# Kernel optimization log

Measured on AMD Instinct MI355X. Metric: run time of the kernel, lower is better.

Reference implementation:

```python
import jax, jax.numpy as jnp
import numpy as np

T, STATE_DIM, ACTION_DIM = 1024, 1024, 64
D, S, H = 2048, 1024, 2048  # deterministic, stochastic, hidden (= embedding_size)


def _lin_init(k, out_dim, in_dim):
    k1, k2 = jax.random.split(k)
    lim = 1.0 / np.sqrt(in_dim)
    w = jax.random.uniform(k1, (out_dim, in_dim), minval=-lim, maxval=lim, dtype=jnp.float32)
    b = jax.random.uniform(k2, (out_dim,), minval=-lim, maxval=lim, dtype=jnp.float32)
    return w, b


def setup_inputs() -> dict:
    key = jax.random.key(0)
    ks = jax.random.split(key, 16)
    enc_w, enc_b = _lin_init(ks[0], H, STATE_DIM)                 # WorldModel.encoder
    dec_w, dec_b = _lin_init(ks[1], STATE_DIM + 2, S + D)         # WorldModel.decoder
    p_enc_w, p_enc_b = _lin_init(ks[2], D, S + ACTION_DIM)        # Prior.encoder
    glim = 1.0 / np.sqrt(D)
    gru_wih = jax.random.uniform(ks[3], (3 * D, D), minval=-glim, maxval=glim, dtype=jnp.float32)
    gru_whh = jax.random.uniform(ks[4], (3 * D, D), minval=-glim, maxval=glim, dtype=jnp.float32)
    gru_b = jax.random.uniform(ks[5], (3 * D,), minval=-glim, maxval=glim, dtype=jnp.float32)
    gru_bn = jax.random.uniform(ks[6], (D,), minval=-glim, maxval=glim, dtype=jnp.float32)
    p_dec1_w, p_dec1_b = _lin_init(ks[7], H, D)                   # Prior.decoder1
    p_dec2_w, p_dec2_b = _lin_init(ks[8], 2 * S, H)               # Prior.decoder2
    q_enc_w, q_enc_b = _lin_init(ks[9], H, D + H)                 # Posterior.encoder
    q_dec_w, q_dec_b = _lin_init(ks[10], 2 * S, H)                # Posterior.decoder
    observation = jax.random.normal(ks[11], (T, STATE_DIM), dtype=jnp.float32)
    actions = jax.random.normal(ks[12], (T, ACTION_DIM), dtype=jnp.float32)
    noise = jax.random.normal(ks[13], (T, S), dtype=jnp.float32)  # reparam eps for posterior sample
    return dict(observation=observation, actions=actions, noise=noise,
                enc_w=enc_w, enc_b=enc_b, dec_w=dec_w, dec_b=dec_b,
                p_enc_w=p_enc_w, p_enc_b=p_enc_b,
                gru_wih=gru_wih, gru_whh=gru_whh, gru_b=gru_b, gru_bn=gru_bn,
                p_dec1_w=p_dec1_w, p_dec1_b=p_dec1_b, p_dec2_w=p_dec2_w, p_dec2_b=p_dec2_b,
                q_enc_w=q_enc_w, q_enc_b=q_enc_b, q_dec_w=q_dec_w, q_dec_b=q_dec_b)


def reference(observation, actions, noise, enc_w, enc_b, dec_w, dec_b,
              p_enc_w, p_enc_b, gru_wih, gru_whh, gru_b, gru_bn,
              p_dec1_w, p_dec1_b, p_dec2_w, p_dec2_b,
              q_enc_w, q_enc_b, q_dec_w, q_dec_b):
    elu = jax.nn.elu
    # obs embeddings: [T, H]
    emb = elu(observation @ enc_w.T + enc_b)

    def step(carry, inp):
        stoch_prev, det_prev = carry
        e, act, eps = inp
        # Prior: encoder -> GRU -> decoder1 -> decoder2
        x = elu(p_enc_w @ jnp.concatenate([stoch_prev, act]) + p_enc_b)  # [D]
        ig = gru_wih @ x + gru_b
        hg = gru_whh @ det_prev
        ir, iz, inw = jnp.split(ig, 3)
        hr, hz, hn = jnp.split(hg, 3)
        r = jax.nn.sigmoid(ir + hr)
        z = jax.nn.sigmoid(iz + hz)
        n = jnp.tanh(inw + r * (hn + gru_bn))
        det = n + z * (det_prev - n)                                     # GRU hidden [D]
        y = elu(p_dec1_w @ det + p_dec1_b)
        y = p_dec2_w @ y + p_dec2_b
        pmu, pstd = jnp.split(y, 2)
        pstd = jax.nn.softplus(pstd) + 0.1
        # Posterior on (det, embedding)
        q = elu(q_enc_w @ jnp.concatenate([det, e]) + q_enc_b)
        q = q_dec_w @ q + q_dec_b
        qmu, qstd = jnp.split(q, 2)
        qstd = jax.nn.softplus(qstd) + 0.1
        stoch = qmu + qstd * eps                                         # Normal sample (reparam)
        return (stoch, det), (stoch, det, qmu, qstd, pmu, pstd)

    init = (jnp.zeros(S, observation.dtype), jnp.zeros(D, observation.dtype))
    _, (stoch, det, qmu, qstd, pmu, pstd) = jax.lax.scan(step, init, (emb, actions, noise))
    states_flat = jnp.concatenate([stoch, det], axis=-1)                  # [T, S+D]
    outs = states_flat @ dec_w.T + dec_b                                  # [T, state_dim+2]
    return stoch, det, outs, qmu, qstd, pmu, pstd


if __name__ == '__main__':
    out = reference(**setup_inputs())
    for o in out:
        print(o.shape)
```

## Files before the change

kernel.cpp:

```cpp
#include <hip/hip_runtime.h>
#include <cstdint>
#include <cstddef>

#define T_STEPS 1024
#define S_DIM   1024
#define A_DIM   64
#define D_DIM   2048
#define H_DIM   2048
#define NWG     256
#define NTHR    512

typedef unsigned short ushort_t;

__device__ __forceinline__ float eluf(float v)      { return v > 0.f ? v : expm1f(v); }
__device__ __forceinline__ float softplusf(float v) { return v > 20.f ? v : log1pf(expf(v)); }
__device__ __forceinline__ float sigmoidf_(float v) { return 1.f / (1.f + expf(-v)); }

__device__ __forceinline__ float wave_reduce(float v) {
  #pragma unroll
  for (int off = 32; off > 0; off >>= 1) v += __shfl_xor(v, off, 64);
  return v;
}

__device__ __forceinline__ float2 bf2(unsigned u) {
  float2 r;
  r.x = __uint_as_float(u << 16);
  r.y = __uint_as_float(u & 0xffff0000u);
  return r;
}
__device__ __forceinline__ ushort_t f2bf_rne(float f) {
  unsigned u = __float_as_uint(f);
  u += 0x7fffu + ((u >> 16) & 1u);
  return (ushort_t)(u >> 16);
}

#define LD_PIN_U4(dst, addr) \
  asm volatile("global_load_dwordx4 %0, %1, off" : "=v"(dst) : "v"(addr))

__device__ __forceinline__ void st_val(float* p, float v) {
  __hip_atomic_store((unsigned*)p, __float_as_uint(v),
                     __ATOMIC_RELAXED, __HIP_MEMORY_SCOPE_AGENT);
}
__device__ __forceinline__ void st_flag(unsigned* p, unsigned g) {
  __hip_atomic_store(p, g, __ATOMIC_RELAXED, __HIP_MEMORY_SCOPE_AGENT);
}

__device__ __forceinline__ void poll_flags(const unsigned* f, unsigned g, int lane) {
  const unsigned* p0 = f + (lane * 4 + 0) * 16;
  const unsigned* p1 = f + (lane * 4 + 1) * 16;
  const unsigned* p2 = f + (lane * 4 + 2) * 16;
  const unsigned* p3 = f + (lane * 4 + 3) * 16;
  for (;;) {
    unsigned a, b, c, d;
    asm volatile("global_load_dword %0, %4, off sc1\n\t"
                 "global_load_dword %1, %5, off sc1\n\t"
                 "global_load_dword %2, %6, off sc1\n\t"
                 "global_load_dword %3, %7, off sc1\n\t"
                 "s_waitcnt vmcnt(0)"
                 : "=v"(a), "=v"(b), "=v"(c), "=v"(d)
                 : "v"(p0), "v"(p1), "v"(p2), "v"(p3) : "memory");
    if (__all(a >= g && b >= g && c >= g && d >= g)) return;
    __builtin_amdgcn_s_sleep(1);
  }
}

__device__ __forceinline__ void bulk4(const float* __restrict__ src, int i4,
                                      float* __restrict__ lds) {
  float4 v;
  asm volatile("global_load_dwordx4 %0, %1, off sc1\n\ts_waitcnt vmcnt(0)"
               : "=v"(v) : "v"(src + i4) : "memory");
  *(float4*)(lds + i4) = v;
}

__global__ void init_flags(unsigned* f) {
  #pragma unroll
  for (int i = 0; i < 64; ++i) f[i * 256 + threadIdx.x] = 0u;
}

__global__ __launch_bounds__(256) void pack_lin(
    const float* __restrict__ src, unsigned* __restrict__ dst,
    int src_ld, int lc, size_t total_u32)
{
  for (size_t u = (size_t)blockIdx.x * 256 + threadIdx.x; u < total_u32;
       u += (size_t)gridDim.x * 256) {
    const size_t pos = u * 2;
    const size_t row = pos >> lc;
    const int    col = (int)(pos & (((size_t)1 << lc) - 1));
    const float2 v = *(const float2*)(src + row * src_ld + col);
    dst[u] = (unsigned)f2bf_rne(v.x) | ((unsigned)f2bf_rne(v.y) << 16);
  }
}

__global__ __launch_bounds__(256) void pack_swz(
    const float* __restrict__ src, unsigned* __restrict__ dst,
    int src_ld, int lc, size_t total2)
{
  for (size_t u = (size_t)blockIdx.x * 256 + threadIdx.x; u < total2;
       u += (size_t)gridDim.x * 256) {
    const size_t pos = u * 2;
    const size_t row = pos >> lc;
    const int pcol  = (int)(pos & (((size_t)1 << lc) - 1));
    const int chunk = pcol >> 9;
    const int off   = pcol & 511;
    const int l     = off >> 3;
    const int p     = (off >> 1) & 3;
    const float2 v  = *(const float2*)(src + row * src_ld + chunk * 512 + p * 128 + l * 2);
    dst[u] = (unsigned)f2bf_rne(v.x) | ((unsigned)f2bf_rne(v.y) << 16);
  }
}

__device__ __forceinline__ float chunk_dot(const uint4 w, const float* vchunk, int lane) {
  float acc = 0.f; float2 p, a;
  a = *(const float2*)(vchunk + lane * 2 +   0); p = bf2(w.x); acc += p.x*a.x + p.y*a.y;
  a = *(const float2*)(vchunk + lane * 2 + 128); p = bf2(w.y); acc += p.x*a.x + p.y*a.y;
  a = *(const float2*)(vchunk + lane * 2 + 256); p = bf2(w.z); acc += p.x*a.x + p.y*a.y;
  a = *(const float2*)(vchunk + lane * 2 + 384); p = bf2(w.w); acc += p.x*a.x + p.y*a.y;
  return acc;
}

__global__ __launch_bounds__(NTHR) void rssm_seq(
    const float* __restrict__ pre_act, const float* __restrict__ pre_e,
    unsigned* __restrict__ flags,
    float* __restrict__ sv_vals,
    float* __restrict__ xv,  float* __restrict__ dv, float* __restrict__ qv,
    const unsigned* __restrict__ wps_lin,
    const unsigned* __restrict__ wih_lin,
    const ushort_t* __restrict__ whh_swz,
    const ushort_t* __restrict__ wqe_swz,
    const ushort_t* __restrict__ wqd_swz,
    const float* __restrict__ gru_b, const float* __restrict__ gru_bn,
    const float* __restrict__ q_dec_b, const float* __restrict__ noise,
    float* __restrict__ stoch_out, float* __restrict__ det_out,
    float* __restrict__ qmu_out, float* __restrict__ qstd_out)
{
  __shared__ float    xs[2048];
  __shared__ float    ds[2048];
  __shared__ float    qs[2048];
  __shared__ float    sp[1024];
  __shared__ float    part4[8];
  __shared__ unsigned wps_l[8 * 512];
  __shared__ unsigned wih_l[24 * 1024];

  const int tid  = threadIdx.x;
  const int wv   = tid >> 6;
  const int lane = tid & 63;
  const int bid  = blockIdx.x;
  const int r0   = bid * 8;
  unsigned* flag1 = flags;
  unsigned* flag2 = flags + 256 * 16;
  unsigned* flag3 = flags + 512 * 16;
  unsigned* flag4 = flags + 768 * 16;

  #pragma unroll
  for (int i = 0; i < 8; ++i) {
    const int idx = i * NTHR + tid;
    const int row = idx >> 9, u = idx & 511;
    wps_l[idx] = wps_lin[((size_t)(r0 + row) << 9) | u];
  }
  #pragma unroll
  for (int i = 0; i < 48; ++i) {
    const int idx = i * NTHR + tid;
    const int gr = idx >> 10, u = idx & 1023;
    const int g = gr >> 3, rr = gr & 7;
    wih_l[idx] = wih_lin[((size_t)(g * 2048 + r0 + rr) << 10) | u];
  }

  uint4 w2h[12];
  uint4 w3[4];
  uint4 w4[4];
  {
    const size_t i = (size_t)(r0 + wv);
    #pragma unroll
    for (int g = 0; g < 3; ++g) {
      const uint4* wr = (const uint4*)(whh_swz + (i + (size_t)g * 2048) * 2048);
      #pragma unroll
      for (int c = 0; c < 4; ++c) LD_PIN_U4(w2h[g * 4 + c], wr + c * 64 + lane);
    }
    const uint4* we = (const uint4*)(wqe_swz + i * 2048);
    #pragma unroll
    for (int c = 0; c < 4; ++c) LD_PIN_U4(w3[c], we + c * 64 + lane);
    const int jg = bid * 4 + (wv & 3), sel = wv >> 2;
    const uint4* wd = (const uint4*)(wqd_swz + (size_t)(jg + sel * 1024) * 2048);
    #pragma unroll
    for (int c = 0; c < 4; ++c) LD_PIN_U4(w4[c], wd + c * 64 + lane);
    asm volatile("s_waitcnt vmcnt(0)" ::: "memory");
  }

  float gb_r = 0.f, gb_z = 0.f, gb_n = 0.f, gbn = 0.f;
  if (lane == 0) {
    gb_r = gru_b[r0 + wv];
    gb_z = gru_b[r0 + wv + 2048];
    gb_n = gru_b[r0 + wv + 4096];
    gbn  = gru_bn[r0 + wv];
  }
  float qdb_m = 0.f, qdb_s = 0.f;
  if (tid < 4) {
    qdb_m = q_dec_b[bid * 4 + tid];
    qdb_s = q_dec_b[bid * 4 + tid + 1024];
  }

  if (tid < 256) ((float4*)sp)[tid] = float4{0.f, 0.f, 0.f, 0.f};
  ((float4*)ds)[tid] = float4{0.f, 0.f, 0.f, 0.f};
  __syncthreads();

  for (int t = 0; t < T_STEPS; ++t) {
    const unsigned gen = (unsigned)(t + 1);
    float pa = 0.f, pe = 0.f;
    if (lane == 0) {
      pa = pre_act[(size_t)t * D_DIM + r0 + wv];
      pe = pre_e  [(size_t)t * H_DIM + r0 + wv];
    }

    if (t > 0) {
      if (wv == 0) poll_flags(flag4, (unsigned)t, lane);
      __syncthreads();
      if (tid < 256) bulk4(sv_vals, 4 * tid, sp);
    }
    __syncthreads();

    {
      const unsigned* wrow = wps_l + (wv << 9);
      float acc = 0.f;
      #pragma unroll
      for (int c = 0; c < 2; ++c)
        #pragma unroll
        for (int p = 0; p < 4; ++p) {
          const float2 a = *(const float2*)(sp + c * 512 + p * 128 + lane * 2);
          const float2 w = bf2(wrow[c * 256 + p * 64 + lane]);
          acc += w.x * a.x + w.y * a.y;
        }
      acc = wave_reduce(acc);
      if (lane == 0) st_val(xv + r0 + wv, eluf(acc + pa));
      asm volatile("s_waitcnt vmcnt(0)" ::: "memory");
    }
    __syncthreads();
    if (tid == 0) st_flag(flag1 + bid * 16, gen);

    float h0 = 0.f, h1 = 0.f, h2 = 0.f;
    #pragma unroll
    for (int c = 0; c < 4; ++c) {
      #pragma unroll
      for (int p = 0; p < 4; ++p) {
        const float2 dvv = *(const float2*)(ds + c * 512 + p * 128 + lane * 2);
        const unsigned u0 = (p == 0) ? w2h[c].x     : (p == 1) ? w2h[c].y     : (p == 2) ? w2h[c].z     : w2h[c].w;
        const unsigned u1 = (p == 0) ? w2h[4 + c].x : (p == 1) ? w2h[4 + c].y : (p == 2) ? w2h[4 + c].z : w2h[4 + c].w;
        const unsigned u2 = (p == 0) ? w2h[8 + c].x : (p == 1) ? w2h[8 + c].y : (p == 2) ? w2h[8 + c].z : w2h[8 + c].w;
        float2 w;
        w = bf2(u0); h0 += w.x * dvv.x + w.y * dvv.y;
        w = bf2(u1); h1 += w.x * dvv.x + w.y * dvv.y;
        w = bf2(u2); h2 += w.x * dvv.x + w.y * dvv.y;
      }
    }
    h0 = wave_reduce(h0); h1 = wave_reduce(h1); h2 = wave_reduce(h2);

    if (wv == 0) poll_flags(flag1, gen, lane);
    __syncthreads();
    bulk4(xv, 4 * tid, xs);
    __syncthreads();
    {
      const unsigned* wg0 = wih_l + wv * 1024;
      const unsigned* wg1 = wg0 + 8192;
      const unsigned* wg2 = wg1 + 8192;
      float a0 = 0.f, a1 = 0.f, a2 = 0.f;
      #pragma unroll
      for (int c = 0; c < 4; ++c) {
        #pragma unroll
        for (int p = 0; p < 4; ++p) {
          const float2 xvv = *(const float2*)(xs + c * 512 + p * 128 + lane * 2);
          const int wi = c * 256 + p * 64 + lane;
          float2 w;
          w = bf2(wg0[wi]); a0 += w.x * xvv.x + w.y * xvv.y;
          w = bf2(wg1[wi]); a1 += w.x * xvv.x + w.y * xvv.y;
          w = bf2(wg2[wi]); a2 += w.x * xvv.x + w.y * xvv.y;
        }
      }
      a0 = wave_reduce(a0); a1 = wave_reduce(a1); a2 = wave_reduce(a2);
      if (lane == 0) {
        const float r_ = sigmoidf_(a0 + gb_r + h0);
        const float z_ = sigmoidf_(a1 + gb_z + h1);
        const float n_ = tanhf(a2 + gb_n + r_ * (h2 + gbn));
        const float det_v = n_ + z_ * (ds[r0 + wv] - n_);
        st_val(dv + r0 + wv, det_v);
        det_out[(size_t)t * D_DIM + r0 + wv] = det_v;
      }
      asm volatile("s_waitcnt vmcnt(0)" ::: "memory");
    }
    __syncthreads();
    if (tid == 0) st_flag(flag2 + bid * 16, gen);

    if (wv == 0) poll_flags(flag2, gen, lane);
    __syncthreads();
    bulk4(dv, 4 * tid, ds);
    __syncthreads();
    {
      float acc = 0.f;
      #pragma unroll
      for (int c = 0; c < 4; ++c) acc += chunk_dot(w3[c], ds + c * 512, lane);
      acc = wave_reduce(acc);
      if (lane == 0) st_val(qv + r0 + wv, eluf(acc + pe));
      asm volatile("s_waitcnt vmcnt(0)" ::: "memory");
    }
    __syncthreads();
    if (tid == 0) st_flag(flag3 + bid * 16, gen);

    if (wv == 0) poll_flags(flag3, gen, lane);
    __syncthreads();
    bulk4(qv, 4 * tid, qs);
    __syncthreads();
    {
      float acc = 0.f;
      #pragma unroll
      for (int c = 0; c < 4; ++c) acc += chunk_dot(w4[c], qs + c * 512, lane);
      acc = wave_reduce(acc);
      if (lane == 0) part4[wv] = acc;
    }
    __syncthreads();
    if (tid < 4) {
      const int j = bid * 4 + tid;
      const float qm  = part4[tid] + qdb_m;
      const float qsd = softplusf(part4[tid + 4] + qdb_s) + 0.1f;
      const float sv  = qm + qsd * noise[(size_t)t * S_DIM + j];
      qmu_out  [(size_t)t * S_DIM + j] = qm;
      qstd_out [(size_t)t * S_DIM + j] = qsd;
      stoch_out[(size_t)t * S_DIM + j] = sv;
      st_val(sv_vals + j, sv);
    }
    if (wv == 0) {
      asm volatile("s_waitcnt vmcnt(0)" ::: "memory");
      if (lane == 0) st_flag(flag4 + bid * 16, gen);
    }
  }
}

template <int ACT>
__global__ __launch_bounds__(256) void gemm_xwT(
    const float* __restrict__ X1, int ldx1,
    const float* __restrict__ X2, int ldx2, int ksplit,
    const float* __restrict__ W, int ldw, int woff,
    const float* __restrict__ bias,
    float* __restrict__ C, int ldc,
    int M, int N, int K)
{
  __shared__ float Xs[16][132];
  __shared__ float Ws[16][68];
  const int tid = threadIdx.x;
  const int tx = tid & 15;
  const int ty = tid >> 4;
  const int m0 = blockIdx.y * 128, n0 = blockIdx.x * 64;
  const int xrow = tid >> 1;
  const int xk8  = (tid & 1) * 8;
  const int wrow = tid & 63;
  const int wk4  = (tid >> 6) * 4;
  float acc[8][4] = {};
  for (int k0 = 0; k0 < K; k0 += 16) {
    {
      const int m = m0 + xrow;
      #pragma unroll
      for (int q = 0; q < 2; ++q) {
        const int k = k0 + xk8 + q * 4;
        float4 v = float4{0.f, 0.f, 0.f, 0.f};
        if (m < M) {
          v = (k < ksplit) ? *(const float4*)(X1 + (size_t)m * ldx1 + k)
                           : *(const float4*)(X2 + (size_t)m * ldx2 + (k - ksplit));
        }
        Xs[xk8 + q * 4 + 0][xrow] = v.x;
        Xs[xk8 + q * 4 + 1][xrow] = v.y;
        Xs[xk8 + q * 4 + 2][xrow] = v.z;
        Xs[xk8 + q * 4 + 3][xrow] = v.w;
      }
      const int n = n0 + wrow;
      float4 wv = float4{0.f, 0.f, 0.f, 0.f};
      if (n < N) wv = *(const float4*)(W + (size_t)n * ldw + woff + k0 + wk4);
      Ws[wk4 + 0][wrow] = wv.x;
      Ws[wk4 + 1][wrow] = wv.y;
      Ws[wk4 + 2][wrow] = wv.z;
      Ws[wk4 + 3][wrow] = wv.w;
    }
    __syncthreads();
    #pragma unroll
    for (int kk = 0; kk < 16; ++kk) {
      const float4 a0 = *(const float4*)(&Xs[kk][ty * 8]);
      const float4 a1 = *(const float4*)(&Xs[kk][ty * 8 + 4]);
      const float4 b  = *(const float4*)(&Ws[kk][tx * 4]);
      const float av[8] = {a0.x, a0.y, a0.z, a0.w, a1.x, a1.y, a1.z, a1.w};
      const float bv[4] = {b.x, b.y, b.z, b.w};
      #pragma unroll
      for (int i = 0; i < 8; ++i)
        #pragma unroll
        for (int j = 0; j < 4; ++j)
          acc[i][j] += av[i] * bv[j];
    }
    __syncthreads();
  }
  #pragma unroll
  for (int i = 0; i < 8; ++i) {
    const int m = m0 + ty * 8 + i;
    if (m >= M) continue;
    #pragma unroll
    for (int j = 0; j < 4; ++j) {
      const int n = n0 + tx * 4 + j;
      if (n >= N) continue;
      float v = acc[i][j] + bias[n];
      if (ACT == 1) v = eluf(v);
      if (ACT == 2) {
        if (n < 1024) C[(size_t)m * 1024 + n] = v;
        else          C[(size_t)m * 1024 + (n - 1024) + 1024 * 1024] = softplusf(v) + 0.1f;
      } else {
        C[(size_t)m * ldc + n] = v;
      }
    }
  }
}

extern "C" void kernel_launch(void* const* d_in, const int* in_sizes, int n_in,
                              void* d_out, int out_size, void* d_ws, size_t ws_size,
                              hipStream_t stream)
{
  const float* obs      = (const float*)d_in[0];
  const float* acts     = (const float*)d_in[1];
  const float* noise    = (const float*)d_in[2];
  const float* enc_w    = (const float*)d_in[3];
  const float* enc_b    = (const float*)d_in[4];
  const float* dec_w    = (const float*)d_in[5];
  const float* dec_b    = (const float*)d_in[6];
  const float* p_enc_w  = (const float*)d_in[7];
  const float* p_enc_b  = (const float*)d_in[8];
  const float* gru_wih  = (const float*)d_in[9];
  const float* gru_whh  = (const float*)d_in[10];
  const float* gru_b    = (const float*)d_in[11];
  const float* gru_bn   = (const float*)d_in[12];
  const float* p_dec1_w = (const float*)d_in[13];
  const float* p_dec1_b = (const float*)d_in[14];
  const float* p_dec2_w = (const float*)d_in[15];
  const float* p_dec2_b = (const float*)d_in[16];
  const float* q_enc_w  = (const float*)d_in[17];
  const float* q_enc_b  = (const float*)d_in[18];
  const float* q_dec_w  = (const float*)d_in[19];
  const float* q_dec_b  = (const float*)d_in[20];

  float* out   = (float*)d_out;
  float* stoch = out;
  float* det   = out + 1048576;
  float* outs  = out + 3145728;
  float* qmu   = out + 4196352;
  float* qstd  = out + 5244928;
  float* pmu   = out + 6293504;

  unsigned* flags = (unsigned*)outs;
  float* sv_vals = outs + 16384;
  float* xv      = sv_vals + 1024;
  float* dvv     = xv + 2048;
  float* qvv     = dvv + 2048;

  float* ws       = (float*)d_ws;
  float* pre_act  = ws;
  float* pre_e    = ws + 2097152;
  float* emb      = ws + 4194304;
  ushort_t* wpack = (ushort_t*)(ws + 6299648);
  ushort_t* wps_lin = wpack;
  ushort_t* wih_lin = wps_lin + 2097152;
  ushort_t* whh_swz = wih_lin + 12582912;
  ushort_t* wqe_swz = whh_swz + 12582912;
  ushort_t* wqd_swz = wqe_swz + 4194304;

  init_flags<<<dim3(1), dim3(256), 0, stream>>>(flags);

  pack_lin<<<dim3(1024), dim3(256), 0, stream>>>(p_enc_w, (unsigned*)wps_lin, 1088, 10, 1048576);
  pack_lin<<<dim3(1024), dim3(256), 0, stream>>>(gru_wih, (unsigned*)wih_lin, 2048, 11, 6291456);
  pack_swz<<<dim3(1024), dim3(256), 0, stream>>>(gru_whh, (unsigned*)whh_swz, 2048, 11, 6291456);
  pack_swz<<<dim3(1024), dim3(256), 0, stream>>>(q_enc_w, (unsigned*)wqe_swz, 4096, 11, 2097152);
  pack_swz<<<dim3(1024), dim3(256), 0, stream>>>(q_dec_w, (unsigned*)wqd_swz, 2048, 11, 2097152);

  dim3 blk(256);
  gemm_xwT<0><<<dim3(32, 8), blk, 0, stream>>>(
      acts, 64, acts, 64, 64, p_enc_w, 1088, 1024, p_enc_b, pre_act, 2048, 1024, 2048, 64);
  gemm_xwT<1><<<dim3(32, 8), blk, 0, stream>>>(
      obs, 1024, obs, 1024, 1024, enc_w, 1024, 0, enc_b, emb, 2048, 1024, 2048, 1024);
  gemm_xwT<0><<<dim3(32, 8), blk, 0, stream>>>(
      emb, 2048, emb, 2048, 2048, q_enc_w, 4096, 2048, q_enc_b, pre_e, 2048, 1024, 2048, 2048);

  rssm_seq<<<dim3(NWG), dim3(NTHR), 0, stream>>>(
      pre_act, pre_e, flags, sv_vals, xv, dvv, qvv,
      (const unsigned*)wps_lin, (const unsigned*)wih_lin,
      whh_swz, wqe_swz, wqd_swz,
      gru_b, gru_bn, q_dec_b, noise, stoch, det, qmu, qstd);

  gemm_xwT<1><<<dim3(32, 8), blk, 0, stream>>>(
      det, 2048, det, 2048, 2048, p_dec1_w, 2048, 0, p_dec1_b, emb, 2048, 1024, 2048, 2048);
  gemm_xwT<2><<<dim3(32, 8), blk, 0, stream>>>(
      emb, 2048, emb, 2048, 2048, p_dec2_w, 2048, 0, p_dec2_b, pmu, 1024, 1024, 2048, 2048);
  gemm_xwT<0><<<dim3(17, 8), blk, 0, stream>>>(
      stoch, 1024, det, 2048, 1024, dec_w, 3072, 0, dec_b, outs, 1026, 1024, 1026, 3072);
}
```

Before: 17.18 ms.

## Tag exchanged values with generation counters to drop store-wait fences

Each value exchanged between workgroups is now stored as a 64-bit record that packs the float with a generation tag. Consumers spin on the records themselves until every tag matches, instead of relying only on the flag. This removes the s_waitcnt vmcnt(0) drains the producers used to do before raising their flags. The old per-stage flag polls are still there, so the main saving is the producer-side fences, paid for with twice the exchange bytes and per-element spin loops.

```diff
diff --git a/kernel.cpp b/kernel.cpp
--- a/kernel.cpp
+++ b/kernel.cpp
@@ -11,6 +11,7 @@
 #define NTHR    512
 
 typedef unsigned short ushort_t;
+typedef unsigned long long u64;
 
 __device__ __forceinline__ float eluf(float v)      { return v > 0.f ? v : expm1f(v); }
 __device__ __forceinline__ float softplusf(float v) { return v > 20.f ? v : log1pf(expf(v)); }
@@ -37,9 +38,12 @@
 #define LD_PIN_U4(dst, addr) \
   asm volatile("global_load_dwordx4 %0, %1, off" : "=v"(dst) : "v"(addr))
 
-__device__ __forceinline__ void st_val(float* p, float v) {
-  __hip_atomic_store((unsigned*)p, __float_as_uint(v),
-                     __ATOMIC_RELAXED, __HIP_MEMORY_SCOPE_AGENT);
+__device__ __forceinline__ void st_rec(u64* p, float v, unsigned g) {
+  const u64 r = (u64)__float_as_uint(v) | ((u64)g << 32);
+  __hip_atomic_store(p, r, __ATOMIC_RELAXED, __HIP_MEMORY_SCOPE_AGENT);
+}
+__device__ __forceinline__ u64 ld_rec(const u64* p) {
+  return __hip_atomic_load(p, __ATOMIC_RELAXED, __HIP_MEMORY_SCOPE_AGENT);
 }
 __device__ __forceinline__ void st_flag(unsigned* p, unsigned g) {
   __hip_atomic_store(p, g, __ATOMIC_RELAXED, __HIP_MEMORY_SCOPE_AGENT);
@@ -64,17 +68,44 @@
   }
 }
 
-__device__ __forceinline__ void bulk4(const float* __restrict__ src, int i4,
-                                      float* __restrict__ lds) {
-  float4 v;
-  asm volatile("global_load_dwordx4 %0, %1, off sc1\n\ts_waitcnt vmcnt(0)"
-               : "=v"(v) : "v"(src + i4) : "memory");
-  *(float4*)(lds + i4) = v;
-}
-
-__global__ void init_flags(unsigned* f) {
+__device__ __forceinline__ void poll_pair(const u64* __restrict__ q0,
+                                          const u64* __restrict__ q1,
+                                          unsigned g, uint4& a, uint4& b) {
+  int spins = 0;
+  for (;;) {
+    asm volatile("global_load_dwordx4 %0, %2, off sc1\n\t"
+                 "global_load_dwordx4 %1, %3, off sc1\n\t"
+                 "s_waitcnt vmcnt(0)"
+                 : "=v"(a), "=v"(b) : "v"(q0), "v"(q1) : "memory");
+    if (__all(a.y == g && a.w == g && b.y == g && b.w == g)) return;
+    if (++spins > 4096) {
+      const u64 c0 = ld_rec(q0), c1 = ld_rec(q0 + 1);
+      const u64 c2 = ld_rec(q1), c3 = ld_rec(q1 + 1);
+      a.x = (unsigned)c0; a.y = (unsigned)(c0 >> 32);
+      a.z = (unsigned)c1; a.w = (unsigned)(c1 >> 32);
+      b.x = (unsigned)c2; b.y = (unsigned)(c2 >> 32);
+      b.z = (unsigned)c3; b.w = (unsigned)(c3 >> 32);
+      if (__all(a.y == g && a.w == g && b.y == g && b.w == g)) return;
+    }
+    __builtin_amdgcn_s_sleep(1);
+  }
+}
+
+__device__ __forceinline__ void poll4c(const u64* __restrict__ base, int i4,
+                                       unsigned g, float* __restrict__ lds) {
+  uint4 a, b;
+  poll_pair(base + i4, base + i4 + 2, g, a, b);
+  float4 out;
+  out.x = __uint_as_float(a.x);
+  out.y = __uint_as_float(a.z);
+  out.z = __uint_as_float(b.x);
+  out.w = __uint_as_float(b.z);
+  *(float4*)(lds + i4) = out;
+}
+
+__global__ void init_sync(unsigned* f) {
   #pragma unroll
-  for (int i = 0; i < 64; ++i) f[i * 256 + threadIdx.x] = 0u;
+  for (int i = 0; i < 120; ++i) f[i * 256 + threadIdx.x] = 0u;
 }
 
 __global__ __launch_bounds__(256) void pack_lin(
@@ -121,8 +152,8 @@
 __global__ __launch_bounds__(NTHR) void rssm_seq(
     const float* __restrict__ pre_act, const float* __restrict__ pre_e,
     unsigned* __restrict__ flags,
-    float* __restrict__ sv_vals,
-    float* __restrict__ xv,  float* __restrict__ dv, float* __restrict__ qv,
+    u64* __restrict__ rec_s,
+    u64* __restrict__ rec_x,  u64* __restrict__ rec_d, u64* __restrict__ rec_q,
     const unsigned* __restrict__ wps_lin,
     const unsigned* __restrict__ wih_lin,
     const ushort_t* __restrict__ whh_swz,
@@ -204,6 +235,7 @@
   __syncthreads();
 
   for (int t = 0; t < T_STEPS; ++t) {
+    const unsigned gb  = (unsigned)(t * 4);
     const unsigned gen = (unsigned)(t + 1);
     float pa = 0.f, pe = 0.f;
     if (lane == 0) {
@@ -214,7 +246,7 @@
     if (t > 0) {
       if (wv == 0) poll_flags(flag4, (unsigned)t, lane);
       __syncthreads();
-      if (tid < 256) bulk4(sv_vals, 4 * tid, sp);
+      if (tid < 256) poll4c(rec_s, 4 * tid, gb, sp);
     }
     __syncthreads();
 
@@ -230,8 +262,7 @@
           acc += w.x * a.x + w.y * a.y;
         }
       acc = wave_reduce(acc);
-      if (lane == 0) st_val(xv + r0 + wv, eluf(acc + pa));
-      asm volatile("s_waitcnt vmcnt(0)" ::: "memory");
+      if (lane == 0) st_rec(rec_x + r0 + wv, eluf(acc + pa), gb + 1);
     }
     __syncthreads();
     if (tid == 0) st_flag(flag1 + bid * 16, gen);
@@ -255,7 +286,7 @@
 
     if (wv == 0) poll_flags(flag1, gen, lane);
     __syncthreads();
-    bulk4(xv, 4 * tid, xs);
+    poll4c(rec_x, 4 * tid, gb + 1, xs);
     __syncthreads();
     {
       const unsigned* wg0 = wih_l + wv * 1024;
@@ -280,32 +311,30 @@
         const float z_ = sigmoidf_(a1 + gb_z + h1);
         const float n_ = tanhf(a2 + gb_n + r_ * (h2 + gbn));
         const float det_v = n_ + z_ * (ds[r0 + wv] - n_);
-        st_val(dv + r0 + wv, det_v);
+        st_rec(rec_d + r0 + wv, det_v, gb + 2);
         det_out[(size_t)t * D_DIM + r0 + wv] = det_v;
       }
-      asm volatile("s_waitcnt vmcnt(0)" ::: "memory");
     }
     __syncthreads();
     if (tid == 0) st_flag(flag2 + bid * 16, gen);
 
     if (wv == 0) poll_flags(flag2, gen, lane);
     __syncthreads();
-    bulk4(dv, 4 * tid, ds);
+    poll4c(rec_d, 4 * tid, gb + 2, ds);
     __syncthreads();
     {
       float acc = 0.f;
       #pragma unroll
       for (int c = 0; c < 4; ++c) acc += chunk_dot(w3[c], ds + c * 512, lane);
       acc = wave_reduce(acc);
-      if (lane == 0) st_val(qv + r0 + wv, eluf(acc + pe));
-      asm volatile("s_waitcnt vmcnt(0)" ::: "memory");
+      if (lane == 0) st_rec(rec_q + r0 + wv, eluf(acc + pe), gb + 3);
     }
     __syncthreads();
     if (tid == 0) st_flag(flag3 + bid * 16, gen);
 
     if (wv == 0) poll_flags(flag3, gen, lane);
     __syncthreads();
-    bulk4(qv, 4 * tid, qs);
+    poll4c(rec_q, 4 * tid, gb + 3, qs);
     __syncthreads();
     {
       float acc = 0.f;
@@ -323,12 +352,9 @@
       qmu_out  [(size_t)t * S_DIM + j] = qm;
       qstd_out [(size_t)t * S_DIM + j] = qsd;
       stoch_out[(size_t)t * S_DIM + j] = sv;
-      st_val(sv_vals + j, sv);
-    }
-    if (wv == 0) {
-      asm volatile("s_waitcnt vmcnt(0)" ::: "memory");
-      if (lane == 0) st_flag(flag4 + bid * 16, gen);
-    }
+      st_rec(rec_s + j, sv, gb + 4);
+    }
+    if (wv == 0 && lane == 0) st_flag(flag4 + bid * 16, gen);
   }
 }
 
@@ -447,10 +473,10 @@
   float* pmu   = out + 6293504;
 
   unsigned* flags = (unsigned*)outs;
-  float* sv_vals = outs + 16384;
-  float* xv      = sv_vals + 1024;
-  float* dvv     = xv + 2048;
-  float* qvv     = dvv + 2048;
+  u64* rec_s = (u64*)(outs + 16384);
+  u64* rec_x = rec_s + 1024;
+  u64* rec_d = rec_x + 2048;
+  u64* rec_q = rec_d + 2048;
 
   float* ws       = (float*)d_ws;
   float* pre_act  = ws;
@@ -463,7 +489,7 @@
   ushort_t* wqe_swz = whh_swz + 12582912;
   ushort_t* wqd_swz = wqe_swz + 4194304;
 
-  init_flags<<<dim3(1), dim3(256), 0, stream>>>(flags);
+  init_sync<<<dim3(1), dim3(256), 0, stream>>>(flags);
 
   pack_lin<<<dim3(1024), dim3(256), 0, stream>>>(p_enc_w, (unsigned*)wps_lin, 1088, 10, 1048576);
   pack_lin<<<dim3(1024), dim3(256), 0, stream>>>(gru_wih, (unsigned*)wih_lin, 2048, 11, 6291456);
@@ -480,7 +506,7 @@
       emb, 2048, emb, 2048, 2048, q_enc_w, 4096, 2048, q_enc_b, pre_e, 2048, 1024, 2048, 2048);
 
   rssm_seq<<<dim3(NWG), dim3(NTHR), 0, stream>>>(
-      pre_act, pre_e, flags, sv_vals, xv, dvv, qvv,
+      pre_act, pre_e, flags, rec_s, rec_x, rec_d, rec_q,
       (const unsigned*)wps_lin, (const unsigned*)wih_lin,
       whh_swz, wqe_swz, wqd_swz,
       gru_b, gru_bn, q_dec_b, noise, stoch, det, qmu, qstd);
```

After: 18.01 ms. 4.8% more time.
